# Kernel tuning notes

Measured on AMD Instinct MI355X. Metric: run time of the kernel, lower is better.

## Reference

```python
import jax, jax.numpy as jnp
import numpy as np

THRESHOLD = 0.9
EPS = 1e-12


def setup_inputs() -> dict:
    key = jax.random.key(0)
    ks = jax.random.split(key, 7)
    B, D_in, H1, H2, D_out = 8192, 256, 512, 256, 64
    # torch Linear default init ~ U(-1/sqrt(fan_in), 1/sqrt(fan_in)); randn scaled is fine as a stand-in
    def lin(k, out_f, in_f):
        return jax.random.normal(k, (out_f, in_f), dtype=jnp.float32) / np.sqrt(in_f)
    return {
        "x": jax.random.normal(ks[0], (B, D_in), dtype=jnp.float32),
        "W1": lin(ks[1], H1, D_in),
        "b1": jax.random.normal(ks[2], (H1,), dtype=jnp.float32) * 0.01,
        "W2": lin(ks[3], H2, H1),
        "b2": jax.random.normal(ks[4], (H2,), dtype=jnp.float32) * 0.01,
        "W3": lin(ks[5], D_out, H2),
        "b3": jax.random.normal(ks[6], (D_out,), dtype=jnp.float32) * 0.01,
    }


def reference(x, W1, b1, W2, b2, W3, b3):
    # MLP: Linear -> Tanh -> Linear -> Tanh -> Linear (no tanh on last)
    h1 = jnp.tanh(x @ W1.T + b1)          # [B, 512]
    h2 = jnp.tanh(h1 @ W2.T + b2)         # [B, 256]
    out = h2 @ W3.T + b3                  # [B, 64]

    # Pairwise state fidelity: (normalized dot)^2, thresholded adjacency (diag excluded)
    norms = jnp.linalg.norm(out, axis=-1, keepdims=True)  # [B, 1]
    normed = out / (norms + EPS)
    fid = (normed @ normed.T) ** 2                         # [B, B]
    adj = (fid >= THRESHOLD).astype(out.dtype)
    B = out.shape[0]
    adj = adj * (1.0 - jnp.eye(B, dtype=out.dtype))        # no self-edges (i < j pairs only)

    return adj @ out                                       # [B, 64]
```

## Files before the change

### kernel.cpp

```cpp
#include <hip/hip_runtime.h>
#include <hip/hip_bf16.h>
#include <math.h>

#define B_ROWS 8192
#define D_IN   256
#define H1_DIM 512
#define H2_DIM 256
#define D_OUT  64
#define EPSF   1e-12f
#define THRESH 0.9f
#define BAND_LO 0.89f
#define BAND_HI 0.91f

typedef __attribute__((ext_vector_type(8))) short short8;
typedef __attribute__((ext_vector_type(4))) float f32x4;

__device__ inline float tanh_fast(float xx) {
  const float ax = fabsf(xx);
  const float t = __expf(-2.0f * ax);
  const float r = (1.0f - t) / (1.0f + t);
  return xx < 0.0f ? -r : r;
}

__device__ inline void splitf8(float4 a, float4 b, short8& h, short8& m) {
  float v[8] = {a.x, a.y, a.z, a.w, b.x, b.y, b.z, b.w};
  short h8[8], m8[8];
#pragma unroll
  for (int e = 0; e < 8; ++e) {
    __hip_bfloat16 hb = __float2bfloat16(v[e]);
    float hf = __bfloat162float(hb);
    __hip_bfloat16 mb = __float2bfloat16(v[e] - hf);
    h8[e] = *(short*)&hb;
    m8[e] = *(short*)&mb;
  }
  h = *(short8*)h8;
  m = *(short8*)m8;
}

__device__ inline void rd8_swz(const float* buf, int S, int row, int kl,
                               float4& a, float4& b) {
  const int xr = (row & 7) << 2;
  a = *(const float4*)&buf[(row * S + kl) ^ xr];
  b = *(const float4*)&buf[(row * S + kl + 4) ^ xr];
}

__device__ inline void pack8(const float* __restrict__ src, short* __restrict__ dh,
                             short* __restrict__ dm, int t, int C, int lgq) {
  const int lane = t & 63;
  const int g = t >> 6;
  const int q = g & ((1 << lgq) - 1);
  const int I = g >> lgq;
  const int row = I * 16 + (lane & 15);
  const int k0 = q * 32 + ((lane >> 4) << 3);
  const float* p = src + (size_t)row * C + k0;
  short8 hh, mm;
  splitf8(*(const float4*)p, *(const float4*)(p + 4), hh, mm);
  *(short8*)(dh + (size_t)t * 8) = hh;
  *(short8*)(dm + (size_t)t * 8) = mm;
}

__global__ __launch_bounds__(256)
void wpack(const float* __restrict__ W1, const float* __restrict__ W2,
           const float* __restrict__ W3,
           short* w1h, short* w1m, short* w2h, short* w2m,
           short* w3h, short* w3m) {
  const int b = blockIdx.x, tid = threadIdx.x;
  if (b < 64)        pack8(W1, w1h, w1m, b * 256 + tid, 256, 3);
  else if (b < 128)  pack8(W2, w2h, w2m, (b - 64) * 256 + tid, 512, 4);
  else               pack8(W3, w3h, w3m, (b - 128) * 256 + tid, 256, 3);
}

__global__ __launch_bounds__(512, 4)
void fused_mlp16(const float* __restrict__ x,
                 const short* __restrict__ w1h, const short* __restrict__ w1m,
                 const float* __restrict__ b1,
                 const short* __restrict__ w2h, const short* __restrict__ w2m,
                 const float* __restrict__ b2,
                 const short* __restrict__ w3h, const short* __restrict__ w3m,
                 const float* __restrict__ b3,
                 float* __restrict__ out, short* __restrict__ vph,
                 short* __restrict__ vpm) {
  __shared__ __align__(16) char smem[49152];
  short* xph   = (short*)smem;
  short* xpm   = (short*)(smem + 8192);
  float* wbuf1 = (float*)smem;
  float* wbuf3 = (float*)smem;
  short* h1h   = (short*)(smem + 16384);
  short* h1m   = (short*)(smem + 32768);
  float* wbuf2 = (float*)(smem + 16384);
  short* h2ph  = (short*)(smem + 32768);
  short* h2pm  = (short*)(smem + 40960);
  __shared__ float nsum[16];
  __shared__ float invn[16];

  const int tid = threadIdx.x;
  const int wave = tid >> 6, lane = tid & 63;
  const int r0 = blockIdx.x * 16;
  const int col16 = lane & 15;
  const int rbase = (lane >> 4) << 2;

  {
    const int lu = tid & 63, q = tid >> 6;
    const float* p = x + (size_t)(r0 + (lu & 15)) * D_IN + q * 32 + ((lu >> 4) << 3);
    short8 hh, mm;
    splitf8(*(const float4*)p, *(const float4*)(p + 4), hh, mm);
    const int off = (q * 64 + lu) * 8;
    *(short8*)(xph + off) = hh;
    *(short8*)(xpm + off) = mm;
  }
  __syncthreads();

  f32x4 acc1[4];
#pragma unroll
  for (int jj = 0; jj < 4; ++jj) acc1[jj] = (f32x4){0.f, 0.f, 0.f, 0.f};
#pragma unroll 4
  for (int q = 0; q < 8; ++q) {
    const int aoff = (q * 64 + lane) * 8;
    const short8 Ah = *(const short8*)(xph + aoff);
    const short8 Am = *(const short8*)(xpm + aoff);
#pragma unroll
    for (int jj = 0; jj < 4; ++jj) {
      const int boff = (((wave * 4 + jj) * 8 + q) * 64 + lane) * 8;
      const short8 Bh = *(const short8*)(w1h + boff);
      const short8 Bm = *(const short8*)(w1m + boff);
      acc1[jj] = __builtin_amdgcn_mfma_f32_16x16x32_bf16(Ah, Bh, acc1[jj], 0, 0, 0);
      acc1[jj] = __builtin_amdgcn_mfma_f32_16x16x32_bf16(Ah, Bm, acc1[jj], 0, 0, 0);
      acc1[jj] = __builtin_amdgcn_mfma_f32_16x16x32_bf16(Am, Bh, acc1[jj], 0, 0, 0);
    }
  }
  __syncthreads();

  float bv1[4];
#pragma unroll
  for (int jj = 0; jj < 4; ++jj) bv1[jj] = b1[(wave * 4 + jj) * 16 + col16];
#pragma unroll
  for (int h = 0; h < 2; ++h) {
    if ((wave >> 2) == h) {
#pragma unroll
      for (int jj = 0; jj < 4; ++jj)
#pragma unroll
        for (int r = 0; r < 4; ++r) {
          const int row = rbase + r;
          const int col = ((wave & 3) * 4 + jj) * 16 + col16;
          wbuf1[(row * 256 + col) ^ ((row & 7) << 2)] = tanh_fast(acc1[jj][r] + bv1[jj]);
        }
    }
    __syncthreads();
    {
      const int lu = tid & 63, ql = tid >> 6;
      const int row = lu & 15, kl = ql * 32 + ((lu >> 4) << 3);
      float4 a, b;
      rd8_swz(wbuf1, 256, row, kl, a, b);
      short8 hh, mm;
      splitf8(a, b, hh, mm);
      const int off = ((h * 8 + ql) * 64 + lu) * 8;
      *(short8*)(h1h + off) = hh;
      *(short8*)(h1m + off) = mm;
    }
    __syncthreads();
  }

  f32x4 acc2[2];
#pragma unroll
  for (int jj = 0; jj < 2; ++jj) acc2[jj] = (f32x4){0.f, 0.f, 0.f, 0.f};
#pragma unroll 4
  for (int q = 0; q < 16; ++q) {
    const int aoff = (q * 64 + lane) * 8;
    const short8 Ah = *(const short8*)(h1h + aoff);
    const short8 Am = *(const short8*)(h1m + aoff);
#pragma unroll
    for (int jj = 0; jj < 2; ++jj) {
      const int boff = (((wave * 2 + jj) * 16 + q) * 64 + lane) * 8;
      const short8 Bh = *(const short8*)(w2h + boff);
      const short8 Bm = *(const short8*)(w2m + boff);
      acc2[jj] = __builtin_amdgcn_mfma_f32_16x16x32_bf16(Ah, Bh, acc2[jj], 0, 0, 0);
      acc2[jj] = __builtin_amdgcn_mfma_f32_16x16x32_bf16(Ah, Bm, acc2[jj], 0, 0, 0);
      acc2[jj] = __builtin_amdgcn_mfma_f32_16x16x32_bf16(Am, Bh, acc2[jj], 0, 0, 0);
    }
  }
  __syncthreads();

  {
    float bv2[2];
#pragma unroll
    for (int jj = 0; jj < 2; ++jj) bv2[jj] = b2[(wave * 2 + jj) * 16 + col16];
#pragma unroll
    for (int jj = 0; jj < 2; ++jj)
#pragma unroll
      for (int r = 0; r < 4; ++r) {
        const int row = rbase + r;
        const int col = (wave * 2 + jj) * 16 + col16;
        wbuf2[(row * 256 + col) ^ ((row & 7) << 2)] = tanh_fast(acc2[jj][r] + bv2[jj]);
      }
  }
  __syncthreads();
  {
    const int lu = tid & 63, ql = tid >> 6;
    const int row = lu & 15, kl = ql * 32 + ((lu >> 4) << 3);
    float4 a, b;
    rd8_swz(wbuf2, 256, row, kl, a, b);
    short8 hh, mm;
    splitf8(a, b, hh, mm);
    const int off = (ql * 64 + lu) * 8;
    *(short8*)(h2ph + off) = hh;
    *(short8*)(h2pm + off) = mm;
  }
  __syncthreads();

  if (wave < 4) {
    f32x4 acc3 = (f32x4){0.f, 0.f, 0.f, 0.f};
#pragma unroll 4
    for (int q = 0; q < 8; ++q) {
      const int aoff = (q * 64 + lane) * 8;
      const short8 Ah = *(const short8*)(h2ph + aoff);
      const short8 Am = *(const short8*)(h2pm + aoff);
      const int boff = ((wave * 8 + q) * 64 + lane) * 8;
      const short8 Bh = *(const short8*)(w3h + boff);
      const short8 Bm = *(const short8*)(w3m + boff);
      acc3 = __builtin_amdgcn_mfma_f32_16x16x32_bf16(Ah, Bh, acc3, 0, 0, 0);
      acc3 = __builtin_amdgcn_mfma_f32_16x16x32_bf16(Ah, Bm, acc3, 0, 0, 0);
      acc3 = __builtin_amdgcn_mfma_f32_16x16x32_bf16(Am, Bh, acc3, 0, 0, 0);
    }
    const float bv3 = b3[wave * 16 + col16];
#pragma unroll
    for (int r = 0; r < 4; ++r) {
      const int row = rbase + r;
      const int col = wave * 16 + col16;
      wbuf3[(row * 64 + col) ^ ((row & 7) << 2)] = acc3[r] + bv3;
    }
  }
  __syncthreads();

  if (tid < 256) {
    const int row = tid >> 4, c4 = (tid & 15) * 4;
    const float4 a = *(const float4*)&wbuf3[(row * 64 + c4) ^ ((row & 7) << 2)];
    float s = a.x * a.x + a.y * a.y + a.z * a.z + a.w * a.w;
    s += __shfl_xor(s, 1, 64);
    s += __shfl_xor(s, 2, 64);
    s += __shfl_xor(s, 4, 64);
    s += __shfl_xor(s, 8, 64);
    if ((tid & 15) == 0) nsum[row] = s;
  }
  __syncthreads();
  if (tid < 16) invn[tid] = 1.0f / (sqrtf(nsum[tid]) + EPSF);
  __syncthreads();

  if (tid < 256) {
    const int row = tid >> 4, c4 = (tid & 15) * 4;
    *(float4*)(out + (size_t)(r0 + row) * D_OUT + c4) =
        *(const float4*)&wbuf3[(row * 64 + c4) ^ ((row & 7) << 2)];
  }
  if (tid < 128) {
    const int lu = tid & 63, ql = tid >> 6;
    const int row = lu & 15, kl = ql * 32 + ((lu >> 4) << 3);
    const float sc = invn[row];
    float4 a, b;
    rd8_swz(wbuf3, 64, row, kl, a, b);
    a.x *= sc; a.y *= sc; a.z *= sc; a.w *= sc;
    b.x *= sc; b.y *= sc; b.z *= sc; b.w *= sc;
    short8 hh, mm;
    splitf8(a, b, hh, mm);
    const size_t off = (((size_t)blockIdx.x * 2 + ql) * 64 + lu) * 8;
    *(short8*)(vph + off) = hh;
    *(short8*)(vpm + off) = mm;
  }
}

__global__ __launch_bounds__(256, 4)
void gram_lds(const short* __restrict__ vph, const short* __restrict__ vpm,
              const float* __restrict__ out, float* __restrict__ resp) {
  __shared__ __align__(16) short lAh[4 * 1024];
  __shared__ __align__(16) float acc[64 * 64];
  const int tid = threadIdx.x;
  const int wave = tid >> 6, lane = tid & 63;
  const int I = blockIdx.x;
  const int sl = blockIdx.y;
  const int i0 = I * 64;
  const int jbase = sl * 1024;

#pragma unroll
  for (int u = 0; u < 4; ++u)
    *(float4*)&acc[(u * 256 + tid) * 4] = make_float4(0.f, 0.f, 0.f, 0.f);

  {
    const size_t base = (size_t)I * 4096;
#pragma unroll
    for (int u = 0; u < 2; ++u) {
      const int item = wave * 2 + u;
      __builtin_amdgcn_global_load_lds(
          (const __attribute__((address_space(1))) void*)(vph + base + item * 512 + lane * 8),
          (__attribute__((address_space(3))) void*)(lAh + item * 512), 16, 0, 0);
    }
  }
  __syncthreads();

  short8 Bh0, Bh1;
  {
    const short* jb = vph + (size_t)((jbase >> 4) + wave) * 1024;
    Bh0 = *(const short8*)(jb + lane * 8);
    Bh1 = *(const short8*)(jb + 512 + lane * 8);
  }

  for (int u = 0; u < 16; ++u) {
    const int jt = u * 4 + wave;
    const int j0 = jbase + jt * 16;
    short8 Bn0, Bn1;
    if (u < 15) {
      const short* jn = vph + (size_t)((jbase >> 4) + jt + 4) * 1024;
      Bn0 = *(const short8*)(jn + lane * 8);
      Bn1 = *(const short8*)(jn + 512 + lane * 8);
    }

    f32x4 g[4];
#pragma unroll
    for (int it = 0; it < 4; ++it) g[it] = (f32x4){0.f, 0.f, 0.f, 0.f};
#pragma unroll
    for (int it = 0; it < 4; ++it) {
      const short8 A0 = *(const short8*)(lAh + it * 1024 + lane * 8);
      g[it] = __builtin_amdgcn_mfma_f32_16x16x32_bf16(A0, Bh0, g[it], 0, 0, 0);
    }
#pragma unroll
    for (int it = 0; it < 4; ++it) {
      const short8 A1 = *(const short8*)(lAh + it * 1024 + 512 + lane * 8);
      g[it] = __builtin_amdgcn_mfma_f32_16x16x32_bf16(A1, Bh1, g[it], 0, 0, 0);
    }

    bool band = false;
#pragma unroll
    for (int it = 0; it < 4; ++it)
#pragma unroll
      for (int r = 0; r < 4; ++r) {
        const float f = g[it][r] * g[it][r];
        band = band || (f > BAND_LO && f < BAND_HI);
      }
    if (__any(band)) {
      const short* jm = vpm + (size_t)((jbase >> 4) + jt) * 1024;
      const short8 Bm0 = *(const short8*)(jm + lane * 8);
      const short8 Bm1 = *(const short8*)(jm + 512 + lane * 8);
      f32x4 g2a[4], g2b[4];
#pragma unroll
      for (int it = 0; it < 4; ++it) {
        g2a[it] = (f32x4){0.f, 0.f, 0.f, 0.f};
        g2b[it] = (f32x4){0.f, 0.f, 0.f, 0.f};
      }
#pragma unroll
      for (int it = 0; it < 4; ++it) {
        const short8 A0 = *(const short8*)(lAh + it * 1024 + lane * 8);
        const short8 A1 = *(const short8*)(lAh + it * 1024 + 512 + lane * 8);
        g2a[it] = __builtin_amdgcn_mfma_f32_16x16x32_bf16(A0, Bm0, g2a[it], 0, 0, 0);
        g2a[it] = __builtin_amdgcn_mfma_f32_16x16x32_bf16(A1, Bm1, g2a[it], 0, 0, 0);
        const size_t abase = (size_t)(I * 4 + it) * 1024;
        const short8 Am0 = *(const short8*)(vpm + abase + lane * 8);
        const short8 Am1 = *(const short8*)(vpm + abase + 512 + lane * 8);
        g2b[it] = __builtin_amdgcn_mfma_f32_16x16x32_bf16(Am0, Bh0, g2b[it], 0, 0, 0);
        g2b[it] = __builtin_amdgcn_mfma_f32_16x16x32_bf16(Am1, Bh1, g2b[it], 0, 0, 0);
      }
#pragma unroll
      for (int it = 0; it < 4; ++it)
#pragma unroll
        for (int r = 0; r < 4; ++r)
          g[it][r] += (g2a[it][r] + g2b[it][r]);
    }

    const int jtg = (jbase >> 4) + jt;
#pragma unroll
    for (int it = 0; it < 4; ++it) {
      const bool diag = (I * 4 + it) == jtg;
#pragma unroll
      for (int r = 0; r < 4; ++r) {
        unsigned long long m = __ballot(g[it][r] * g[it][r] >= THRESH);
        if (diag) m &= ~(0x1000010000100001ull << r);
        while (m) {
          const int s = __builtin_ctzll(m);
          m &= m - 1;
          const float v = out[(size_t)(j0 + (s & 15)) * D_OUT + lane];
          atomicAdd(&acc[(it * 16 + ((s >> 4) << 2) + r) * 64 + lane], v);
        }
      }
    }
    Bh0 = Bn0;
    Bh1 = Bn1;
  }
  __syncthreads();

  float* dst = resp + ((size_t)sl * B_ROWS + i0) * D_OUT;
#pragma unroll
  for (int u = 0; u < 4; ++u) {
    const int e = u * 256 + tid;
    *(float4*)&dst[e * 4] = *(const float4*)&acc[e * 4];
  }
}

__global__ __launch_bounds__(256)
void reduce8(const float4* __restrict__ resp, float4* __restrict__ res) {
  const int idx = blockIdx.x * 256 + threadIdx.x;
  float4 a = resp[idx];
#pragma unroll
  for (int s = 1; s < 8; ++s) {
    const float4 b = resp[(size_t)s * (B_ROWS * D_OUT / 4) + idx];
    a.x += b.x; a.y += b.y; a.z += b.z; a.w += b.w;
  }
  res[idx] = a;
}

#define MB (1024 * 1024)
#define KB 1024

extern "C" void kernel_launch(void* const* d_in, const int* in_sizes, int n_in,
                              void* d_out, int out_size, void* d_ws, size_t ws_size,
                              hipStream_t stream) {
  const float* x  = (const float*)d_in[0];
  const float* W1 = (const float*)d_in[1];
  const float* b1 = (const float*)d_in[2];
  const float* W2 = (const float*)d_in[3];
  const float* b2 = (const float*)d_in[4];
  const float* W3 = (const float*)d_in[5];
  const float* b3 = (const float*)d_in[6];
  float* res = (float*)d_out;

  char* ws = (char*)d_ws;
  float* out = (float*)(ws);
  short* vph = (short*)(ws + 2 * MB);
  short* vpm = (short*)(ws + 3 * MB);
  short* w1h = (short*)(ws + 4 * MB);
  short* w1m = (short*)(ws + 4 * MB + 256 * KB);
  short* w2h = (short*)(ws + 4 * MB + 512 * KB);
  short* w2m = (short*)(ws + 4 * MB + 768 * KB);
  short* w3h = (short*)(ws + 5 * MB);
  short* w3m = (short*)(ws + 5 * MB + 32 * KB);
  float* resp = (float*)(ws + 6 * MB);

  wpack<<<136, 256, 0, stream>>>(W1, W2, W3, w1h, w1m, w2h, w2m, w3h, w3m);
  fused_mlp16<<<512, 512, 0, stream>>>(x, w1h, w1m, b1, w2h, w2m, b2,
                                       w3h, w3m, b3, out, vph, vpm);
  gram_lds<<<dim3(128, 8), 256, 0, stream>>>(vph, vpm, out, resp);
  reduce8<<<dim3(B_ROWS * D_OUT / 4 / 256), 256, 0, stream>>>(
      (const float4*)resp, (float4*)res);
}
```

Baseline: 133.0 us.

## Always compute three-pass split-bf16 Gram with A tiles held in registers

The Gram kernel now always runs the hi*hi + hi*lo + lo*hi split-bf16 MFMA products, replacing the conditional band check that added correction terms only near the threshold. The A tiles, both hi and lo parts, are loaded once into registers instead of staged through LDS. This removes the warp-divergent correction branch, the extra global loads of A-lo inside it, and the LDS traffic. In exchange it triples MFMA work per tile, drops the B-tile software prefetch, and raises register pressure.

```diff
diff --git a/kernel.cpp b/kernel.cpp
--- a/kernel.cpp
+++ b/kernel.cpp
@@ -9,8 +9,6 @@
 #define D_OUT  64
 #define EPSF   1e-12f
 #define THRESH 0.9f
-#define BAND_LO 0.89f
-#define BAND_HI 0.91f
 
 typedef __attribute__((ext_vector_type(8))) short short8;
 typedef __attribute__((ext_vector_type(4))) float f32x4;
@@ -267,9 +265,8 @@
 }
 
 __global__ __launch_bounds__(256, 4)
-void gram_lds(const short* __restrict__ vph, const short* __restrict__ vpm,
-              const float* __restrict__ out, float* __restrict__ resp) {
-  __shared__ __align__(16) short lAh[4 * 1024];
+void gram3p(const short* __restrict__ vph, const short* __restrict__ vpm,
+            const float* __restrict__ out, float* __restrict__ resp) {
   __shared__ __align__(16) float acc[64 * 64];
   const int tid = threadIdx.x;
   const int wave = tid >> 6, lane = tid & 63;
@@ -282,90 +279,53 @@
   for (int u = 0; u < 4; ++u)
     *(float4*)&acc[(u * 256 + tid) * 4] = make_float4(0.f, 0.f, 0.f, 0.f);
 
-  {
-    const size_t base = (size_t)I * 4096;
-#pragma unroll
-    for (int u = 0; u < 2; ++u) {
-      const int item = wave * 2 + u;
-      __builtin_amdgcn_global_load_lds(
-          (const __attribute__((address_space(1))) void*)(vph + base + item * 512 + lane * 8),
-          (__attribute__((address_space(3))) void*)(lAh + item * 512), 16, 0, 0);
-    }
-  }
-  __syncthreads();
-
-  short8 Bh0, Bh1;
-  {
-    const short* jb = vph + (size_t)((jbase >> 4) + wave) * 1024;
-    Bh0 = *(const short8*)(jb + lane * 8);
-    Bh1 = *(const short8*)(jb + 512 + lane * 8);
-  }
+  short8 Ah[4][2], Am[4][2];
+#pragma unroll
+  for (int it = 0; it < 4; ++it) {
+    const size_t abase = (size_t)(I * 4 + it) * 1024;
+    Ah[it][0] = *(const short8*)(vph + abase + lane * 8);
+    Ah[it][1] = *(const short8*)(vph + abase + 512 + lane * 8);
+    Am[it][0] = *(const short8*)(vpm + abase + lane * 8);
+    Am[it][1] = *(const short8*)(vpm + abase + 512 + lane * 8);
+  }
+  __syncthreads();
 
   for (int u = 0; u < 16; ++u) {
     const int jt = u * 4 + wave;
     const int j0 = jbase + jt * 16;
-    short8 Bn0, Bn1;
-    if (u < 15) {
-      const short* jn = vph + (size_t)((jbase >> 4) + jt + 4) * 1024;
-      Bn0 = *(const short8*)(jn + lane * 8);
-      Bn1 = *(const short8*)(jn + 512 + lane * 8);
-    }
+    const int jb = (jbase >> 4) + jt;
+    const short* ph = vph + (size_t)jb * 1024;
+    const short* pm = vpm + (size_t)jb * 1024;
+    const short8 Bh0 = *(const short8*)(ph + lane * 8);
+    const short8 Bh1 = *(const short8*)(ph + 512 + lane * 8);
+    const short8 Bm0 = *(const short8*)(pm + lane * 8);
+    const short8 Bm1 = *(const short8*)(pm + 512 + lane * 8);
 
     f32x4 g[4];
 #pragma unroll
     for (int it = 0; it < 4; ++it) g[it] = (f32x4){0.f, 0.f, 0.f, 0.f};
 #pragma unroll
+    for (int it = 0; it < 4; ++it)
+      g[it] = __builtin_amdgcn_mfma_f32_16x16x32_bf16(Ah[it][0], Bh0, g[it], 0, 0, 0);
+#pragma unroll
+    for (int it = 0; it < 4; ++it)
+      g[it] = __builtin_amdgcn_mfma_f32_16x16x32_bf16(Ah[it][1], Bh1, g[it], 0, 0, 0);
+#pragma unroll
+    for (int it = 0; it < 4; ++it)
+      g[it] = __builtin_amdgcn_mfma_f32_16x16x32_bf16(Ah[it][0], Bm0, g[it], 0, 0, 0);
+#pragma unroll
+    for (int it = 0; it < 4; ++it)
+      g[it] = __builtin_amdgcn_mfma_f32_16x16x32_bf16(Am[it][0], Bh0, g[it], 0, 0, 0);
+#pragma unroll
+    for (int it = 0; it < 4; ++it)
+      g[it] = __builtin_amdgcn_mfma_f32_16x16x32_bf16(Ah[it][1], Bm1, g[it], 0, 0, 0);
+#pragma unroll
+    for (int it = 0; it < 4; ++it)
+      g[it] = __builtin_amdgcn_mfma_f32_16x16x32_bf16(Am[it][1], Bh1, g[it], 0, 0, 0);
+
+#pragma unroll
     for (int it = 0; it < 4; ++it) {
-      const short8 A0 = *(const short8*)(lAh + it * 1024 + lane * 8);
-      g[it] = __builtin_amdgcn_mfma_f32_16x16x32_bf16(A0, Bh0, g[it], 0, 0, 0);
-    }
-#pragma unroll
-    for (int it = 0; it < 4; ++it) {
-      const short8 A1 = *(const short8*)(lAh + it * 1024 + 512 + lane * 8);
-      g[it] = __builtin_amdgcn_mfma_f32_16x16x32_bf16(A1, Bh1, g[it], 0, 0, 0);
-    }
-
-    bool band = false;
-#pragma unroll
-    for (int it = 0; it < 4; ++it)
-#pragma unroll
-      for (int r = 0; r < 4; ++r) {
-        const float f = g[it][r] * g[it][r];
-        band = band || (f > BAND_LO && f < BAND_HI);
-      }
-    if (__any(band)) {
-      const short* jm = vpm + (size_t)((jbase >> 4) + jt) * 1024;
-      const short8 Bm0 = *(const short8*)(jm + lane * 8);
-      const short8 Bm1 = *(const short8*)(jm + 512 + lane * 8);
-      f32x4 g2a[4], g2b[4];
-#pragma unroll
-      for (int it = 0; it < 4; ++it) {
-        g2a[it] = (f32x4){0.f, 0.f, 0.f, 0.f};
-        g2b[it] = (f32x4){0.f, 0.f, 0.f, 0.f};
-      }
-#pragma unroll
-      for (int it = 0; it < 4; ++it) {
-        const short8 A0 = *(const short8*)(lAh + it * 1024 + lane * 8);
-        const short8 A1 = *(const short8*)(lAh + it * 1024 + 512 + lane * 8);
-        g2a[it] = __builtin_amdgcn_mfma_f32_16x16x32_bf16(A0, Bm0, g2a[it], 0, 0, 0);
-        g2a[it] = __builtin_amdgcn_mfma_f32_16x16x32_bf16(A1, Bm1, g2a[it], 0, 0, 0);
-        const size_t abase = (size_t)(I * 4 + it) * 1024;
-        const short8 Am0 = *(const short8*)(vpm + abase + lane * 8);
-        const short8 Am1 = *(const short8*)(vpm + abase + 512 + lane * 8);
-        g2b[it] = __builtin_amdgcn_mfma_f32_16x16x32_bf16(Am0, Bh0, g2b[it], 0, 0, 0);
-        g2b[it] = __builtin_amdgcn_mfma_f32_16x16x32_bf16(Am1, Bh1, g2b[it], 0, 0, 0);
-      }
-#pragma unroll
-      for (int it = 0; it < 4; ++it)
-#pragma unroll
-        for (int r = 0; r < 4; ++r)
-          g[it][r] += (g2a[it][r] + g2b[it][r]);
-    }
-
-    const int jtg = (jbase >> 4) + jt;
-#pragma unroll
-    for (int it = 0; it < 4; ++it) {
-      const bool diag = (I * 4 + it) == jtg;
+      const bool diag = (I * 4 + it) == jb;
 #pragma unroll
       for (int r = 0; r < 4; ++r) {
         unsigned long long m = __ballot(g[it][r] * g[it][r] >= THRESH);
@@ -378,8 +338,6 @@
         }
       }
     }
-    Bh0 = Bn0;
-    Bh1 = Bn1;
   }
   __syncthreads();
 
@@ -433,7 +391,7 @@
   wpack<<<136, 256, 0, stream>>>(W1, W2, W3, w1h, w1m, w2h, w2m, w3h, w3m);
   fused_mlp16<<<512, 512, 0, stream>>>(x, w1h, w1m, b1, w2h, w2m, b2,
                                        w3h, w3m, b3, out, vph, vpm);
-  gram_lds<<<dim3(128, 8), 256, 0, stream>>>(vph, vpm, out, resp);
+  gram3p<<<dim3(128, 8), 256, 0, stream>>>(vph, vpm, out, resp);
   reduce8<<<dim3(B_ROWS * D_OUT / 4 / 256), 256, 0, stream>>>(
       (const float4*)resp, (float4*)res);
 }
```

New measurement: 130.6 us. No clear change (-1.8%).
